# Kernel optimization log

Hardware: AMD Instinct MI355X
Metric: run time of the kernel (lower is better)

Reference implementation:

```python
import jax, jax.numpy as jnp
import numpy as np

DEPTH = 2
DIM = 256
MLP = 1024
B = 2
N = 2048


def setup_inputs() -> dict:
    key = jax.random.key(0)
    ks = jax.random.split(key, 6)
    s = 0.02
    d = DIM
    f32 = jnp.float32
    return {
        "x": jax.random.normal(ks[0], (B, N, d), f32),
        "ln1_g": jnp.ones((DEPTH, d), f32),
        "ln1_b": jnp.zeros((DEPTH, d), f32),
        "Wqkv": (jax.random.normal(ks[1], (DEPTH, d, 3 * d), f32) * s),
        "bqkv": jnp.zeros((DEPTH, 3 * d), f32),
        "Wo": (jax.random.normal(ks[2], (DEPTH, d, d), f32) * s),
        "bo": jnp.zeros((DEPTH, d), f32),
        "ln2_g": jnp.ones((DEPTH, d), f32),
        "ln2_b": jnp.zeros((DEPTH, d), f32),
        "W1": (jax.random.normal(ks[3], (DEPTH, d, MLP), f32) * s),
        "b1": jnp.zeros((DEPTH, MLP), f32),
        "W2": (jax.random.normal(ks[4], (DEPTH, MLP, d), f32) * s),
        "b2": jnp.zeros((DEPTH, d), f32),
        "heads": 8,
    }


def _ln(x, g, b, eps=1e-5):
    m = x.mean(-1, keepdims=True)
    v = ((x - m) ** 2).mean(-1, keepdims=True)
    return (x - m) * jax.lax.rsqrt(v + eps) * g + b


def reference(x, ln1_g, ln1_b, Wqkv, bqkv, Wo, bo, ln2_g, ln2_b, W1, b1, W2, b2, heads):
    b, n, dim = x.shape
    hd = dim // heads
    scale = hd ** -0.5
    depth = Wqkv.shape[0]
    out = x
    # NOTE: faithful to original: `x` is never updated inside the loop,
    # so only the last layer's output is returned.
    for i in range(depth):
        y = _ln(x, ln1_g[i], ln1_b[i])
        qkv = y @ Wqkv[i] + bqkv[i]                      # [b,n,3*dim]
        qkv = qkv.reshape(b, n, 3, heads, hd)
        q, k, v = jnp.moveaxis(qkv, 2, 0)                # each [b,n,h,hd]
        q = q.transpose(0, 2, 1, 3)                      # [b,h,n,hd]
        k = k.transpose(0, 2, 1, 3)
        v = v.transpose(0, 2, 1, 3)
        dots = jnp.einsum('bhid,bhjd->bhij', q, k) * scale
        attn = jax.nn.softmax(dots, axis=-1)
        o = jnp.einsum('bhij,bhjd->bhid', attn, v)       # [b,h,n,hd]
        o = o.transpose(0, 2, 1, 3).reshape(b, n, dim)
        o = o @ Wo[i] + bo[i]
        a = o + x                                        # attn residual
        z = _ln(a, ln2_g[i], ln2_b[i])
        m = jax.nn.gelu(z @ W1[i] + b1[i], approximate=False) @ W2[i] + b2[i]
        out = m + a                                      # mlp residual
    return out
```

## Files before the change

### kernel.cpp

```cpp
#include <hip/hip_runtime.h>
#include <hip/hip_bf16.h>
#include <math.h>

#define DEPTHC 2
#define DIMD   256
#define MLPD   1024
#define BB     2
#define NN     2048
#define HH     8
#define HD     32
#define ROWS   (BB * NN)

typedef __attribute__((ext_vector_type(8))) short bf16x8;
typedef __attribute__((ext_vector_type(4))) float f32x4;

__device__ __forceinline__ short f2bf(float x) {
    union { float f; unsigned u; } c; c.f = x;
    unsigned u = c.u + (0x7fffu + ((c.u >> 16) & 1u));
    return (short)(u >> 16);
}

__global__ __launch_bounds__(256) void prep(
    const float* __restrict__ Wqkv, const float* __restrict__ Wo,
    const float* __restrict__ W1,   const float* __restrict__ W2,
    short* __restrict__ WqkvF, short* __restrict__ WoF,
    short* __restrict__ W1F,   short* __restrict__ W2F,
    const float* __restrict__ x, const float* __restrict__ g,
    const float* __restrict__ be, short* __restrict__ y)
{
    __shared__ short Ts[128][72];

    if (blockIdx.x >= 96) {
        const int wave = threadIdx.x >> 6;
        const int lane = threadIdx.x & 63;
        const int row  = (blockIdx.x - 96) * 4 + wave;
        const int c    = lane * 4;

        const float4 v = *(const float4*)&x[(size_t)row * DIMD + c];
        float s  = v.x + v.y + v.z + v.w;
        float sq = v.x * v.x + v.y * v.y + v.z * v.z + v.w * v.w;
#pragma unroll
        for (int off = 32; off > 0; off >>= 1) {
            s  += __shfl_down(s,  off, 64);
            sq += __shfl_down(sq, off, 64);
        }
        s  = __shfl(s,  0, 64);
        sq = __shfl(sq, 0, 64);

        const float mean = s * (1.f / DIMD);
        const float var  = sq * (1.f / DIMD) - mean * mean;
        const float rstd = rsqrtf(var + 1e-5f);

        const float4 gg = *(const float4*)&g[c];
        const float4 bb = *(const float4*)&be[c];
        short4 ov;
        ov.x = f2bf((v.x - mean) * rstd * gg.x + bb.x);
        ov.y = f2bf((v.y - mean) * rstd * gg.y + bb.y);
        ov.z = f2bf((v.z - mean) * rstd * gg.z + bb.z);
        ov.w = f2bf((v.w - mean) * rstd * gg.w + bb.w);
        *(short4*)&y[(size_t)row * DIMD + c] = ov;
        return;
    }

    int blk = blockIdx.x;
    const float* W; short* WF; int K, N;
    if (blk < 24)      {           W = Wqkv; WF = WqkvF; K = 256;  N = 768;  }
    else if (blk < 32) { blk -= 24; W = Wo;   WF = WoF;   K = 256;  N = 256;  }
    else if (blk < 64) { blk -= 32; W = W1;   WF = W1F;   K = 256;  N = 1024; }
    else               { blk -= 64; W = W2;   WF = W2F;   K = 1024; N = 256;  }
    const int nkc = K >> 7;
    const int bx  = blk / nkc;
    const int kc  = blk % nkc;
    const int n0  = bx * 64;
    const int k0  = kc * 128;

    const int nc  = threadIdx.x & 63;
    const int kr0 = threadIdx.x >> 6;
#pragma unroll
    for (int i = 0; i < 32; ++i) {
        const int kr = kr0 + i * 4;
        Ts[kr][nc] = f2bf(W[(size_t)(k0 + kr) * N + n0 + nc]);
    }
    __syncthreads();

    short* out = WF + ((size_t)bx * nkc + kc) * 8192;
#pragma unroll
    for (int i = 0; i < 4; ++i) {
        const int u    = threadIdx.x + i * 256;
        const int l16  = u & 15;
        const int quad = (u >> 4) & 3;
        const int nt   = (u >> 6) & 3;
        const int ks   = (u >> 8) & 3;
        const int n    = nt * 16 + l16;
        const int kk   = (ks * 4 + quad) * 8;
        bf16x8 v;
#pragma unroll
        for (int j = 0; j < 8; ++j) v[j] = Ts[kk + j][n];
        *(bf16x8*)&out[(size_t)u * 8] = v;
    }
}

template <int K, bool GELU, bool RES, bool OBF, bool VTG>
__global__ __launch_bounds__(256) void gemm_ks(
    const short* __restrict__ A, const short* __restrict__ WF,
    const float* __restrict__ bias, const float* __restrict__ R,
    void* __restrict__ Cv, int N,
    short* __restrict__ qpk, short* __restrict__ kpk, short* __restrict__ vtg)
{
    __shared__ short smem[4][4096];
    __shared__ short vts[64][66];

    const int tid  = threadIdx.x;
    const int w    = tid >> 6;
    const int lane = tid & 63;
    const int quad = lane >> 4;
    const int l16  = lane & 15;
    const int n0   = blockIdx.x * 64;
    const int m0   = blockIdx.y * 64;
    constexpr int NKC   = K / 128;
    constexpr int SLICE = K / 4;
    constexpr int NHC   = SLICE / 64;

    const short* wfb  = WF + (size_t)blockIdx.x * NKC * 8192;
    const short* arow = A + (size_t)(m0 + l16) * K + quad * 8;
    short* reg = smem[w];

    f32x4 acc[4][4] = {};

#pragma unroll
    for (int hc = 0; hc < NHC; ++hc) {
        const int kbase = w * SLICE + hc * 64;
        const short* src = wfb +
            ((size_t)(kbase >> 7) * 1024 + (size_t)((kbase >> 6) & 1) * 512) * 8;
#pragma unroll
        for (int i = 0; i < 8; ++i)
            *(bf16x8*)&reg[(i * 64 + lane) * 8] =
                *(const bf16x8*)&src[(size_t)(i * 64 + lane) * 8];

#pragma unroll
        for (int ksl = 0; ksl < 2; ++ksl) {
            const int kk = kbase + ksl * 32;
            bf16x8 af[4];
#pragma unroll
            for (int mt = 0; mt < 4; ++mt)
                af[mt] = *(const bf16x8*)(arow + (size_t)mt * 16 * K + kk);
#pragma unroll
            for (int nt = 0; nt < 4; ++nt) {
                const bf16x8 bf = *(const bf16x8*)
                    &reg[(((ksl * 4 + nt) * 4 + quad) * 16 + l16) * 8];
#pragma unroll
                for (int mt = 0; mt < 4; ++mt)
                    acc[mt][nt] = __builtin_amdgcn_mfma_f32_16x16x32_bf16(
                        af[mt], bf, acc[mt][nt], 0, 0, 0);
            }
        }
    }

#pragma unroll
    for (int p = 0; p < 2; ++p) {
        __syncthreads();
#pragma unroll
        for (int mtl = 0; mtl < 2; ++mtl)
#pragma unroll
            for (int nt = 0; nt < 4; ++nt)
                *(f32x4*)&smem[w][((mtl * 4 + nt) * 64 + lane) * 8] = acc[2 * p + mtl][nt];
        __syncthreads();
        if ((w >> 1) == p) {
            const int mtl = w & 1;
            const int mt  = 2 * p + mtl;
#pragma unroll
            for (int nt = 0; nt < 4; ++nt) {
                const int idx = ((mtl * 4 + nt) * 64 + lane) * 8;
                const f32x4 s0 = *(const f32x4*)&smem[0][idx];
                const f32x4 s1 = *(const f32x4*)&smem[1][idx];
                const f32x4 s2 = *(const f32x4*)&smem[2][idx];
                const f32x4 s3 = *(const f32x4*)&smem[3][idx];
                const f32x4 s  = (s0 + s1) + (s2 + s3);
                const int col  = n0 + nt * 16 + l16;
                const float bb = bias[col];
#pragma unroll
                for (int r = 0; r < 4; ++r) {
                    const int row = m0 + mt * 16 + quad * 4 + r;
                    float v = s[r] + bb;
                    if (RES)  v += R[(size_t)row * N + col];
                    if (GELU) v = 0.5f * v * (1.f + erff(v * 0.70710678118f));
                    const short bv = f2bf(v);
                    if (VTG) {
                        vts[row - m0][col - n0] = bv;
                    } else if (OBF) {
                        ((short*)Cv)[(size_t)row * N + col] = bv;
                    } else {
                        ((float*)Cv)[(size_t)row * N + col] = v;
                    }
                }
            }
        }
    }

    if (VTG) {
        __syncthreads();
        const int b   = m0 >> 11;
        const int q0v = m0 & (NN - 1);
        if (n0 < 2 * DIMD) {
            short* dstb = (n0 < DIMD) ? qpk : kpk;
            const int bc   = n0 & (DIMD - 1);
            const int tok  = tid >> 2;
            const int dseg = (tid & 3) * 16;
            const int c = bc + dseg;
            const int h = c >> 5;
            const int d = c & 31;
            short tmp[16];
#pragma unroll
            for (int i = 0; i < 16; ++i) tmp[i] = vts[tok][dseg + i];
            short* dst = dstb + ((size_t)(b * HH + h) * NN + q0v + tok) * HD + d;
            *(bf16x8*)dst       = *(const bf16x8*)&tmp[0];
            *(bf16x8*)(dst + 8) = *(const bf16x8*)&tmp[8];
        } else {
            const int vcol = tid >> 2;
            const int tseg = (tid & 3) * 16;
            const int vc   = n0 - 2 * DIMD + vcol;
            const int h    = vc >> 5;
            const int d    = vc & 31;
            short tmp[16];
#pragma unroll
            for (int i = 0; i < 16; ++i) tmp[i] = vts[tseg + i][vcol];
            short* dst = &vtg[((size_t)(b * HH + h) * HD + d) * NN + q0v + tseg];
            *(bf16x8*)dst       = *(const bf16x8*)&tmp[0];
            *(bf16x8*)(dst + 8) = *(const bf16x8*)&tmp[8];
        }
    }
}

__global__ __launch_bounds__(256) void attn_mfma(
    const short* __restrict__ qpk, const short* __restrict__ kpk,
    const short* __restrict__ vtg, short* __restrict__ o)
{
    __shared__ __align__(16) short Ks2[2][64][44];
    __shared__ __align__(16) short Vs2[2][32][72];
    __shared__ __align__(16) short Ps[4][16][72];

    const int tid  = threadIdx.x;
    const int w    = tid >> 6;
    const int lane = tid & 63;
    const int quad = lane >> 4;
    const int l16  = lane & 15;
    const int qw    = w & 1;
    const int kside = w >> 1;
    const int bh   = blockIdx.y;
    const int b    = bh >> 3;
    const int h    = bh & 7;
    const int q0   = blockIdx.x * 32 + qw * 16;

    const float scale = 0.17677669529663689f;
    const float shift = 11.090354888959125f;

    const bf16x8 qfrag =
        *(const bf16x8*)(qpk + ((size_t)bh * NN + q0 + l16) * HD + quad * 8);

    const int side = tid >> 7;
    const int st   = tid & 127;
    const int kr   = st >> 1;
    const int kd   = (st & 1) * 16;
    const int vd   = st >> 2;
    const int vk0  = (st & 3) * 16;

    const short* kgp = kpk + ((size_t)bh * NN + side * 1024 + kr) * HD + kd;
    const short* vgp = vtg + ((size_t)bh * HD + vd) * NN + side * 1024 + vk0;

    f32x4 oacc0 = {0.f, 0.f, 0.f, 0.f};
    f32x4 oacc1 = {0.f, 0.f, 0.f, 0.f};
    float rowsum = 0.f;

    bf16x8 kr0 = *(const bf16x8*)kgp;
    bf16x8 kr1 = *(const bf16x8*)(kgp + 8);
    bf16x8 vr0 = *(const bf16x8*)vgp;
    bf16x8 vr1 = *(const bf16x8*)(vgp + 8);

#pragma unroll 1
    for (int t = 0; t < NN / 128; ++t) {
        __syncthreads();
        *(bf16x8*)&Ks2[side][kr][kd]     = kr0;
        *(bf16x8*)&Ks2[side][kr][kd + 8] = kr1;
        *(bf16x8*)&Vs2[side][vd][vk0]     = vr0;
        *(bf16x8*)&Vs2[side][vd][vk0 + 8] = vr1;
        __syncthreads();

        if (t + 1 < NN / 128) {
            const short* kn = kgp + (size_t)(t + 1) * 64 * HD;
            const short* vn = vgp + (t + 1) * 64;
            kr0 = *(const bf16x8*)kn;
            kr1 = *(const bf16x8*)(kn + 8);
            vr0 = *(const bf16x8*)vn;
            vr1 = *(const bf16x8*)(vn + 8);
        }

        f32x4 s[4];
#pragma unroll
        for (int kt = 0; kt < 4; ++kt) {
            const bf16x8 kf = *(const bf16x8*)&Ks2[kside][kt * 16 + l16][quad * 8];
            f32x4 z = {0.f, 0.f, 0.f, 0.f};
            s[kt] = __builtin_amdgcn_mfma_f32_16x16x32_bf16(kf, qfrag, z, 0, 0, 0);
        }

#pragma unroll
        for (int kt = 0; kt < 4; ++kt) {
            short4 pv;
#pragma unroll
            for (int r = 0; r < 4; ++r) {
                const float p = __expf(fmaf(s[kt][r], scale, -shift));
                rowsum += p;
                union { float f; unsigned u; } cv; cv.f = p;
                ((short*)&pv)[r] = (short)(cv.u >> 16);
            }
            *(short4*)&Ps[w][l16][kt * 16 + quad * 4] = pv;
        }

#pragma unroll
        for (int c = 0; c < 2; ++c) {
            const bf16x8 pf = *(const bf16x8*)&Ps[w][l16][c * 32 + quad * 8];
            const bf16x8 v0 = *(const bf16x8*)&Vs2[kside][l16][c * 32 + quad * 8];
            const bf16x8 v1 = *(const bf16x8*)&Vs2[kside][16 + l16][c * 32 + quad * 8];
            oacc0 = __builtin_amdgcn_mfma_f32_16x16x32_bf16(pf, v0, oacc0, 0, 0, 0);
            oacc1 = __builtin_amdgcn_mfma_f32_16x16x32_bf16(pf, v1, oacc1, 0, 0, 0);
        }
    }

    rowsum += __shfl_xor(rowsum, 16, 64);
    rowsum += __shfl_xor(rowsum, 32, 64);

    float* sc = (float*)&Ks2[0][0][0];
    __syncthreads();
    if (kside == 1) {
        float* o8 = sc + (size_t)(qw * 64 + lane) * 8;
        *(f32x4*)o8       = oacc0;
        *(f32x4*)(o8 + 4) = oacc1;
        if (lane < 16) sc[1024 + qw * 16 + lane] = rowsum;
    }
    __syncthreads();
    if (kside == 0) {
        const float* o8 = sc + (size_t)(qw * 64 + lane) * 8;
        oacc0 += *(const f32x4*)o8;
        oacc1 += *(const f32x4*)(o8 + 4);
        rowsum += sc[1024 + qw * 16 + l16];

#pragma unroll
        for (int r = 0; r < 4; ++r) {
            const float L   = __shfl(rowsum, quad * 4 + r, 16);
            const float inv = 1.f / L;
            const size_t row = (size_t)(b * NN + q0 + quad * 4 + r);
            o[row * DIMD + h * HD + l16]      = f2bf(oacc0[r] * inv);
            o[row * DIMD + h * HD + 16 + l16] = f2bf(oacc1[r] * inv);
        }
    }
}

__global__ __launch_bounds__(1024) void tail_fused(
    const short* __restrict__ obf, const float* __restrict__ x,
    const short* __restrict__ WoF, const float* __restrict__ bo,
    const float* __restrict__ ln2g, const float* __restrict__ ln2b,
    const short* __restrict__ W1F, const float* __restrict__ b1,
    const short* __restrict__ W2F, const float* __restrict__ b2,
    float* __restrict__ out)
{
    __shared__ __align__(16) float aS[16][264];
    __shared__ __align__(16) short zS[16][264];
    __shared__ __align__(16) short mS[16][1032];

    const int tid  = threadIdx.x;
    const int w    = tid >> 6;
    const int lane = tid & 63;
    const int quad = lane >> 4;
    const int l16  = lane & 15;
    const int m0   = blockIdx.x * 16;

    {
        const short* arow   = obf + (size_t)(m0 + l16) * DIMD + quad * 8;
        const short* wchunk = WoF + (size_t)(w >> 2) * 2 * 8192;
        const int ntl = w & 3;
        f32x4 acc = {};
#pragma unroll
        for (int ks = 0; ks < 8; ++ks) {
            const int k = ks * 32;
            const bf16x8 af = *(const bf16x8*)(arow + k);
            const int ub = (k >> 7) * 1024 + ((k >> 5) & 3) * 256 + quad * 16 + l16;
            const bf16x8 bf = *(const bf16x8*)&wchunk[(size_t)(ub + ntl * 64) * 8];
            acc = __builtin_amdgcn_mfma_f32_16x16x32_bf16(af, bf, acc, 0, 0, 0);
        }
        const int col  = w * 16 + l16;
        const float bb = bo[col];
#pragma unroll
        for (int r = 0; r < 4; ++r) {
            const int row = quad * 4 + r;
            aS[row][col] = acc[r] + bb + x[(size_t)(m0 + row) * DIMD + col];
        }
    }
    __syncthreads();

    {
        const int row = w;
        const int c4  = lane * 4;
        const float4 v = *(const float4*)&aS[row][c4];
        float s  = v.x + v.y + v.z + v.w;
        float sq = v.x * v.x + v.y * v.y + v.z * v.z + v.w * v.w;
#pragma unroll
        for (int off = 32; off > 0; off >>= 1) {
            s  += __shfl_xor(s,  off, 64);
            sq += __shfl_xor(sq, off, 64);
        }
        const float mean = s * (1.f / DIMD);
        const float var  = sq * (1.f / DIMD) - mean * mean;
        const float rstd = rsqrtf(var + 1e-5f);
        const float4 gg = *(const float4*)&ln2g[c4];
        const float4 bb = *(const float4*)&ln2b[c4];
        short4 ov;
        ov.x = f2bf((v.x - mean) * rstd * gg.x + bb.x);
        ov.y = f2bf((v.y - mean) * rstd * gg.y + bb.y);
        ov.z = f2bf((v.z - mean) * rstd * gg.z + bb.z);
        ov.w = f2bf((v.w - mean) * rstd * gg.w + bb.w);
        *(short4*)&zS[row][c4] = ov;
    }
    __syncthreads();

    {
        f32x4 acc[4] = {};
#pragma unroll
        for (int ks = 0; ks < 8; ++ks) {
            const int k = ks * 32;
            const bf16x8 af = *(const bf16x8*)&zS[l16][k + quad * 8];
            const int ub = (k >> 7) * 1024 + ((k >> 5) & 3) * 256 + quad * 16 + l16;
#pragma unroll
            for (int nt = 0; nt < 4; ++nt) {
                const bf16x8 bf = *(const bf16x8*)
                    &W1F[(size_t)w * 2 * 8192 + (size_t)(ub + nt * 64) * 8];
                acc[nt] = __builtin_amdgcn_mfma_f32_16x16x32_bf16(af, bf, acc[nt], 0, 0, 0);
            }
        }
#pragma unroll
        for (int nt = 0; nt < 4; ++nt) {
            const int col  = w * 64 + nt * 16 + l16;
            const float bb = b1[col];
#pragma unroll
            for (int r = 0; r < 4; ++r) {
                float v = acc[nt][r] + bb;
                v = 0.5f * v * (1.f + erff(v * 0.70710678118f));
                mS[quad * 4 + r][col] = f2bf(v);
            }
        }
    }
    __syncthreads();

    {
        f32x4 acc = {};
        const short* wchunk = W2F + (size_t)(w >> 2) * 8 * 8192;
        const int ntl = w & 3;
#pragma unroll
        for (int ks = 0; ks < 32; ++ks) {
            const int k = ks * 32;
            const bf16x8 af = *(const bf16x8*)&mS[l16][k + quad * 8];
            const int ub = (k >> 7) * 1024 + ((k >> 5) & 3) * 256 + quad * 16 + l16;
            const bf16x8 bf = *(const bf16x8*)&wchunk[(size_t)(ub + ntl * 64) * 8];
            acc = __builtin_amdgcn_mfma_f32_16x16x32_bf16(af, bf, acc, 0, 0, 0);
        }
        const int col  = w * 16 + l16;
        const float bb = b2[col];
#pragma unroll
        for (int r = 0; r < 4; ++r) {
            const int row = quad * 4 + r;
            out[(size_t)(m0 + row) * DIMD + col] = acc[r] + bb + aS[row][col];
        }
    }
}

extern "C" void kernel_launch(void* const* d_in, const int* in_sizes, int n_in,
                              void* d_out, int out_size, void* d_ws, size_t ws_size,
                              hipStream_t stream)
{
    const int L = DEPTHC - 1;
    const float* x     = (const float*)d_in[0];
    const float* ln1_g = (const float*)d_in[1]  + L * DIMD;
    const float* ln1_b = (const float*)d_in[2]  + L * DIMD;
    const float* Wqkv  = (const float*)d_in[3]  + (size_t)L * DIMD * 3 * DIMD;
    const float* bqkv  = (const float*)d_in[4]  + L * 3 * DIMD;
    const float* Wo    = (const float*)d_in[5]  + (size_t)L * DIMD * DIMD;
    const float* bo    = (const float*)d_in[6]  + L * DIMD;
    const float* ln2_g = (const float*)d_in[7]  + L * DIMD;
    const float* ln2_b = (const float*)d_in[8]  + L * DIMD;
    const float* W1    = (const float*)d_in[9]  + (size_t)L * DIMD * MLPD;
    const float* b1    = (const float*)d_in[10] + L * MLPD;
    const float* W2    = (const float*)d_in[11] + (size_t)L * MLPD * DIMD;
    const float* b2    = (const float*)d_in[12] + L * DIMD;
    float* out = (float*)d_out;

    short* WqkvF = (short*)d_ws;
    short* WoF   = WqkvF + 12 * 2 * 8192;
    short* W1F   = WoF   + 4 * 2 * 8192;
    short* W2F   = W1F   + 16 * 2 * 8192;
    short* ybf   = W2F   + 4 * 8 * 8192;
    short* qpk   = ybf   + (size_t)ROWS * DIMD;
    short* kpk   = qpk   + (size_t)16 * NN * HD;
    short* vtg   = kpk   + (size_t)16 * NN * HD;
    short* obf   = vtg   + (size_t)16 * HD * NN;

    prep<<<96 + ROWS / 4, 256, 0, stream>>>(
        Wqkv, Wo, W1, W2, WqkvF, WoF, W1F, W2F, x, ln1_g, ln1_b, ybf);

    gemm_ks<256, false, false, false, true><<<dim3(12, 64), 256, 0, stream>>>(
        ybf, WqkvF, bqkv, nullptr, nullptr, 3 * DIMD, qpk, kpk, vtg);

    attn_mfma<<<dim3(NN / 32, BB * HH), 256, 0, stream>>>(qpk, kpk, vtg, obf);

    tail_fused<<<ROWS / 16, 1024, 0, stream>>>(
        obf, x, WoF, bo, ln2_g, ln2_b, W1F, b1, W2F, b2, out);
}
```

Baseline: 139.6 us.

## Replace split-K QKV GEMM with per-wave M-split and direct weight loads

The QKV projection GEMM is rewritten so that each of the four waves owns 16 rows of the 64-row tile and runs the full K=256 loop, instead of each wave taking a quarter of K. This removes the shared-memory staging of the weight fragments and the cross-wave reduction with its extra syncs. Weight fragments are now read straight from global memory, and each wave reads all of them, so the same weights are fetched four times per block and L2/L1 pressure rises. The scatter into the Q/K/Vᵀ layouts is unchanged.

```diff
diff --git a/kernel.cpp b/kernel.cpp
--- a/kernel.cpp
+++ b/kernel.cpp
@@ -100,14 +100,11 @@
     }
 }
 
-template <int K, bool GELU, bool RES, bool OBF, bool VTG>
-__global__ __launch_bounds__(256) void gemm_ks(
+__global__ __launch_bounds__(256) void qkv_gemm(
     const short* __restrict__ A, const short* __restrict__ WF,
-    const float* __restrict__ bias, const float* __restrict__ R,
-    void* __restrict__ Cv, int N,
+    const float* __restrict__ bias,
     short* __restrict__ qpk, short* __restrict__ kpk, short* __restrict__ vtg)
 {
-    __shared__ short smem[4][4096];
     __shared__ short vts[64][66];
 
     const int tid  = threadIdx.x;
@@ -117,117 +114,61 @@
     const int l16  = lane & 15;
     const int n0   = blockIdx.x * 64;
     const int m0   = blockIdx.y * 64;
-    constexpr int NKC   = K / 128;
-    constexpr int SLICE = K / 4;
-    constexpr int NHC   = SLICE / 64;
-
-    const short* wfb  = WF + (size_t)blockIdx.x * NKC * 8192;
-    const short* arow = A + (size_t)(m0 + l16) * K + quad * 8;
-    short* reg = smem[w];
-
-    f32x4 acc[4][4] = {};
-
-#pragma unroll
-    for (int hc = 0; hc < NHC; ++hc) {
-        const int kbase = w * SLICE + hc * 64;
-        const short* src = wfb +
-            ((size_t)(kbase >> 7) * 1024 + (size_t)((kbase >> 6) & 1) * 512) * 8;
-#pragma unroll
-        for (int i = 0; i < 8; ++i)
-            *(bf16x8*)&reg[(i * 64 + lane) * 8] =
-                *(const bf16x8*)&src[(size_t)(i * 64 + lane) * 8];
-
-#pragma unroll
-        for (int ksl = 0; ksl < 2; ++ksl) {
-            const int kk = kbase + ksl * 32;
-            bf16x8 af[4];
-#pragma unroll
-            for (int mt = 0; mt < 4; ++mt)
-                af[mt] = *(const bf16x8*)(arow + (size_t)mt * 16 * K + kk);
-#pragma unroll
-            for (int nt = 0; nt < 4; ++nt) {
-                const bf16x8 bf = *(const bf16x8*)
-                    &reg[(((ksl * 4 + nt) * 4 + quad) * 16 + l16) * 8];
-#pragma unroll
-                for (int mt = 0; mt < 4; ++mt)
-                    acc[mt][nt] = __builtin_amdgcn_mfma_f32_16x16x32_bf16(
-                        af[mt], bf, acc[mt][nt], 0, 0, 0);
-            }
-        }
-    }
-
-#pragma unroll
-    for (int p = 0; p < 2; ++p) {
-        __syncthreads();
-#pragma unroll
-        for (int mtl = 0; mtl < 2; ++mtl)
-#pragma unroll
-            for (int nt = 0; nt < 4; ++nt)
-                *(f32x4*)&smem[w][((mtl * 4 + nt) * 64 + lane) * 8] = acc[2 * p + mtl][nt];
-        __syncthreads();
-        if ((w >> 1) == p) {
-            const int mtl = w & 1;
-            const int mt  = 2 * p + mtl;
-#pragma unroll
-            for (int nt = 0; nt < 4; ++nt) {
-                const int idx = ((mtl * 4 + nt) * 64 + lane) * 8;
-                const f32x4 s0 = *(const f32x4*)&smem[0][idx];
-                const f32x4 s1 = *(const f32x4*)&smem[1][idx];
-                const f32x4 s2 = *(const f32x4*)&smem[2][idx];
-                const f32x4 s3 = *(const f32x4*)&smem[3][idx];
-                const f32x4 s  = (s0 + s1) + (s2 + s3);
-                const int col  = n0 + nt * 16 + l16;
-                const float bb = bias[col];
-#pragma unroll
-                for (int r = 0; r < 4; ++r) {
-                    const int row = m0 + mt * 16 + quad * 4 + r;
-                    float v = s[r] + bb;
-                    if (RES)  v += R[(size_t)row * N + col];
-                    if (GELU) v = 0.5f * v * (1.f + erff(v * 0.70710678118f));
-                    const short bv = f2bf(v);
-                    if (VTG) {
-                        vts[row - m0][col - n0] = bv;
-                    } else if (OBF) {
-                        ((short*)Cv)[(size_t)row * N + col] = bv;
-                    } else {
-                        ((float*)Cv)[(size_t)row * N + col] = v;
-                    }
-                }
-            }
-        }
-    }
-
-    if (VTG) {
-        __syncthreads();
-        const int b   = m0 >> 11;
-        const int q0v = m0 & (NN - 1);
-        if (n0 < 2 * DIMD) {
-            short* dstb = (n0 < DIMD) ? qpk : kpk;
-            const int bc   = n0 & (DIMD - 1);
-            const int tok  = tid >> 2;
-            const int dseg = (tid & 3) * 16;
-            const int c = bc + dseg;
-            const int h = c >> 5;
-            const int d = c & 31;
-            short tmp[16];
-#pragma unroll
-            for (int i = 0; i < 16; ++i) tmp[i] = vts[tok][dseg + i];
-            short* dst = dstb + ((size_t)(b * HH + h) * NN + q0v + tok) * HD + d;
-            *(bf16x8*)dst       = *(const bf16x8*)&tmp[0];
-            *(bf16x8*)(dst + 8) = *(const bf16x8*)&tmp[8];
-        } else {
-            const int vcol = tid >> 2;
-            const int tseg = (tid & 3) * 16;
-            const int vc   = n0 - 2 * DIMD + vcol;
-            const int h    = vc >> 5;
-            const int d    = vc & 31;
-            short tmp[16];
-#pragma unroll
-            for (int i = 0; i < 16; ++i) tmp[i] = vts[tseg + i][vcol];
-            short* dst = &vtg[((size_t)(b * HH + h) * HD + d) * NN + q0v + tseg];
-            *(bf16x8*)dst       = *(const bf16x8*)&tmp[0];
-            *(bf16x8*)(dst + 8) = *(const bf16x8*)&tmp[8];
-        }
+
+    const short* wchunk = WF + (size_t)blockIdx.x * 2 * 8192;
+    const short* arow   = A + (size_t)(m0 + w * 16 + l16) * DIMD + quad * 8;
+
+    f32x4 acc[4] = {};
+#pragma unroll
+    for (int ks = 0; ks < 8; ++ks) {
+        const int k = ks * 32;
+        const bf16x8 af = *(const bf16x8*)(arow + k);
+        const int ub = (k >> 7) * 1024 + ((k >> 5) & 3) * 256 + quad * 16 + l16;
+#pragma unroll
+        for (int nt = 0; nt < 4; ++nt) {
+            const bf16x8 bf = *(const bf16x8*)&wchunk[(size_t)(ub + nt * 64) * 8];
+            acc[nt] = __builtin_amdgcn_mfma_f32_16x16x32_bf16(af, bf, acc[nt], 0, 0, 0);
+        }
+    }
+
+#pragma unroll
+    for (int nt = 0; nt < 4; ++nt) {
+        const int col  = n0 + nt * 16 + l16;
+        const float bb = bias[col];
+#pragma unroll
+        for (int r = 0; r < 4; ++r)
+            vts[w * 16 + quad * 4 + r][nt * 16 + l16] = f2bf(acc[nt][r] + bb);
+    }
+    __syncthreads();
+
+    const int b   = m0 >> 11;
+    const int q0v = m0 & (NN - 1);
+    if (n0 < 2 * DIMD) {
+        short* dstb = (n0 < DIMD) ? qpk : kpk;
+        const int bc   = n0 & (DIMD - 1);
+        const int tok  = tid >> 2;
+        const int dseg = (tid & 3) * 16;
+        const int c = bc + dseg;
+        const int h = c >> 5;
+        const int d = c & 31;
+        short tmp[16];
+#pragma unroll
+        for (int i = 0; i < 16; ++i) tmp[i] = vts[tok][dseg + i];
+        short* dst = dstb + ((size_t)(b * HH + h) * NN + q0v + tok) * HD + d;
+        *(bf16x8*)dst       = *(const bf16x8*)&tmp[0];
+        *(bf16x8*)(dst + 8) = *(const bf16x8*)&tmp[8];
+    } else {
+        const int vcol = tid >> 2;
+        const int tseg = (tid & 3) * 16;
+        const int vc   = n0 - 2 * DIMD + vcol;
+        const int h    = vc >> 5;
+        const int d    = vc & 31;
+        short tmp[16];
+#pragma unroll
+        for (int i = 0; i < 16; ++i) tmp[i] = vts[tseg + i][vcol];
+        short* dst = &vtg[((size_t)(b * HH + h) * HD + d) * NN + q0v + tseg];
+        *(bf16x8*)dst       = *(const bf16x8*)&tmp[0];
+        *(bf16x8*)(dst + 8) = *(const bf16x8*)&tmp[8];
     }
 }
 
@@ -504,8 +445,8 @@
     prep<<<96 + ROWS / 4, 256, 0, stream>>>(
         Wqkv, Wo, W1, W2, WqkvF, WoF, W1F, W2F, x, ln1_g, ln1_b, ybf);
 
-    gemm_ks<256, false, false, false, true><<<dim3(12, 64), 256, 0, stream>>>(
-        ybf, WqkvF, bqkv, nullptr, nullptr, 3 * DIMD, qpk, kpk, vtg);
+    qkv_gemm<<<dim3(12, 64), 256, 0, stream>>>(
+        ybf, WqkvF, bqkv, qpk, kpk, vtg);
 
     attn_mfma<<<dim3(NN / 32, BB * HH), 256, 0, stream>>>(qpk, kpk, vtg, obf);
 
```

After: 138.9 us. About the same (-0.5%).
